# Kernel optimization log

Measured on AMD Instinct MI355X. Metric: run time of the kernel, lower is better.

Reference implementation:

```python
import jax, jax.numpy as jnp
import numpy as np

B, C_IN, H, W = 2, 256, 64, 64
D, NH, WS = 128, 8, 8          # embed_dim, num_heads, window_size
N_PTS = 8192
CAP = 256                      # max tokens per window (64 pixels + points, padded)
ODE_STEPS = 4                  # fixed-step RK4 approximating dopri5 on t in [0,1]


def setup_inputs() -> dict:
    key = jax.random.key(0)
    ks = jax.random.split(key, 16)
    p = lambda k, shape, fan: (jax.random.normal(k, shape, jnp.float32) / np.float32(np.sqrt(fan)))
    return {
        "in_image_feat": jax.random.normal(ks[0], (B, C_IN, H, W), jnp.float32),
        "pts_uv": jax.random.randint(ks[1], (N_PTS, 3), 0, 64),
        "pts_feat": jax.random.normal(ks[2], (N_PTS, D), jnp.float32),
        "conv_in_w": p(ks[3], (D, C_IN), C_IN),         # conv256_128 (1x1)
        "conv_in_b": jnp.zeros((D,), jnp.float32),
        "qkv_w": p(ks[4], (3 * D, D), D),               # sptr attn qkv
        "qkv_b": jnp.zeros((3 * D,), jnp.float32),
        "attnproj_w": p(ks[5], (D, D), D),              # sptr attn out proj
        "attnproj_b": jnp.zeros((D,), jnp.float32),
        "ode_w": p(ks[6], (D, D), D),                   # outimagefc128_128_ode
        "ode_b": jnp.zeros((D,), jnp.float32),
        "conv_out_w": p(ks[7], (C_IN, D), D),           # conv128_256 (1x1)
        "conv_out_b": jnp.zeros((C_IN,), jnp.float32),
    }


def _windowed_attention(feat, wid, NW, qkv_w, qkv_b, proj_w, proj_b):
    """Var-length windowed MHSA (sptr.VarLengthMultiheadSA) via pad-to-CAP."""
    T, d = feat.shape
    hd = d // NH
    order = jnp.argsort(wid)                      # stable sort by window id
    wid_s, feat_s = wid[order], feat[order]
    counts = jax.ops.segment_sum(jnp.ones_like(wid), wid, num_segments=NW)
    starts = jnp.cumsum(counts) - counts
    rank = jnp.arange(T) - starts[wid_s]          # within-window position
    valid = rank < CAP
    wid_w = jnp.where(valid, wid_s, NW)           # overflow -> dummy window
    rank_w = jnp.where(valid, rank, 0)
    buf = jnp.zeros((NW + 1, CAP, d), feat.dtype).at[wid_w, rank_w].set(feat_s)
    msk = jnp.zeros((NW + 1, CAP), bool).at[wid_w, rank_w].set(valid)
    qkv = buf @ qkv_w.T + qkv_b                   # [NW+1, CAP, 3d]
    q, k, v = (t.reshape(NW + 1, CAP, NH, hd) for t in jnp.split(qkv, 3, axis=-1))
    scores = jnp.einsum('wqhd,wkhd->whqk', q, k) / np.float32(np.sqrt(hd))
    scores = jnp.where(msk[:, None, None, :], scores, jnp.float32(-1e9))
    attn = jax.nn.softmax(scores, axis=-1)
    o = jnp.einsum('whqk,wkhd->wqhd', attn, v).reshape(NW + 1, CAP, d)
    o = o @ proj_w.T + proj_b
    out_s = jnp.where(valid[:, None], o[wid_w, rank_w], feat_s)
    return jnp.zeros_like(out_s).at[order].set(out_s)  # unsort


def reference(in_image_feat, pts_uv, pts_feat, conv_in_w, conv_in_b,
              qkv_w, qkv_b, attnproj_w, attnproj_b,
              ode_w, ode_b, conv_out_w, conv_out_b):
    b, c, h, w = in_image_feat.shape
    d = conv_in_w.shape[0]
    # 1x1 conv 256->128
    x = jnp.einsum('bchw,ec->bhwe', in_image_feat, conv_in_w) + conv_in_b
    pix_feat = x.reshape(b * h * w, d)
    # pixel uv grid (convert_image_to_uv): flatten order (b, h, w); u=w idx, v=h idx
    vv, uu = jnp.meshgrid(jnp.arange(h), jnp.arange(w), indexing='ij')
    pix_b = jnp.repeat(jnp.arange(b), h * w)
    pix_u = jnp.tile(uu.reshape(-1), b)
    pix_v = jnp.tile(vv.reshape(-1), b)
    # projected point uv (convert_pts_to_uv result, made in-range)
    pts_b = pts_uv[:, 0] % b
    pts_u = pts_uv[:, 1] % w
    pts_v = pts_uv[:, 2] % h
    tok_b = jnp.concatenate([pix_b, pts_b])
    tok_u = jnp.concatenate([pix_u, pts_u])
    tok_v = jnp.concatenate([pix_v, pts_v])
    feat = jnp.concatenate([pix_feat, pts_feat], axis=0)
    nwx, nwy = w // WS, h // WS
    wid = (tok_b * nwy + tok_v // WS) * nwx + tok_u // WS
    NW = b * nwx * nwy
    out = _windowed_attention(feat, wid, NW, qkv_w, qkv_b, attnproj_w, attnproj_b)
    img = out[: b * h * w]
    # fcode branch: odeint(ODEFunc(Linear), t=[0,1]) ~ fixed-step RK4, + residual
    f = lambda y: jax.nn.relu(y @ ode_w.T + ode_b)
    dt = jnp.float32(1.0 / ODE_STEPS)
    y = img
    for _ in range(ODE_STEPS):
        k1 = f(y); k2 = f(y + 0.5 * dt * k1); k3 = f(y + 0.5 * dt * k2); k4 = f(y + dt * k3)
        y = y + (dt / 6.0) * (k1 + 2.0 * k2 + 2.0 * k3 + k4)
    img = y + img
    # 1x1 conv 128->256 back to image layout
    img = img.reshape(b, h, w, d)
    return jnp.einsum('bhwd,cd->bchw', img, conv_out_w) + conv_out_b[None, :, None, None]
```

## Files before the change

kernel.cpp:

```cpp
#include <hip/hip_runtime.h>

typedef short bf16x8 __attribute__((ext_vector_type(8)));
typedef float f32x4 __attribute__((ext_vector_type(4)));

__device__ __forceinline__ float b2f(unsigned short s) {
    union { float f; unsigned u; } x; x.u = ((unsigned)s) << 16; return x.f;
}
__device__ __forceinline__ unsigned short f2b(float f) {
    unsigned u = __float_as_uint(f);
    unsigned r = (u + 0x7fffu + ((u >> 16) & 1u)) >> 16;
    return (unsigned short)r;
}

__global__ __launch_bounds__(256) void cast_k(const float* __restrict__ ciw,
                                              const float* __restrict__ qw,
                                              const float* __restrict__ pw,
                                              const float* __restrict__ ow,
                                              const float* __restrict__ cw,
                                              unsigned short* __restrict__ dst,
                                              int* __restrict__ cnt) {
    if (blockIdx.x == 0 && threadIdx.x < 128) cnt[threadIdx.x] = 0;
    int i = blockIdx.x * 256 + threadIdx.x;
    float v;
    if (i < 32768)        v = ciw[i];
    else if (i < 81920)   v = qw[i - 32768];
    else if (i < 98304)   v = pw[i - 81920];
    else if (i < 114688)  v = ow[i - 98304];
    else                  v = cw[i - 114688];
    dst[i] = f2b(v);
}

__global__ __launch_bounds__(256) void assign_k(const int* __restrict__ uv,
                                                int* __restrict__ cnt,
                                                int* __restrict__ wpts) {
    int i = blockIdx.x * 256 + threadIdx.x;
    if (i >= 8192) return;
    int b = uv[3 * i] & 1;
    int u = uv[3 * i + 1] & 63;
    int v = uv[3 * i + 2] & 63;
    int w = b * 64 + ((v >> 3) << 3) + (u >> 3);
    int slot = atomicAdd(cnt + w, 1);
    if (slot < 192) wpts[w * 192 + slot] = i;
}

__global__ __launch_bounds__(256) void cin_k(const float* __restrict__ in,
                                             const unsigned short* __restrict__ Wm,
                                             const float* __restrict__ bias,
                                             unsigned short* __restrict__ feat) {
    __shared__ unsigned short t[64][65];
    __shared__ unsigned short At[64][264];
    int p0 = blockIdx.x * 64, b = p0 >> 12, hw0 = p0 & 4095;
    int lane = threadIdx.x & 63, quad = threadIdx.x >> 6;
    for (int j = 0; j < 4; ++j) {
        int c0 = j * 64;
#pragma unroll
        for (int i = 0; i < 16; ++i) {
            int c = quad + i * 4;
            t[c][lane] = f2b(in[((size_t)(b * 256 + c0 + c)) * 4096 + hw0 + lane]);
        }
        __syncthreads();
#pragma unroll
        for (int i = 0; i < 16; ++i) {
            int p = quad + i * 4;
            At[p][c0 + lane] = t[lane][p];
        }
        __syncthreads();
    }
    int q = lane & 15, g = lane >> 4;
    int m0 = quad * 16;
    f32x4 acc[8];
#pragma unroll
    for (int tn = 0; tn < 8; ++tn) acc[tn] = (f32x4){0.f, 0.f, 0.f, 0.f};
#pragma unroll
    for (int k0 = 0; k0 < 256; k0 += 32) {
        bf16x8 a = *(const bf16x8*)&At[m0 + q][k0 + g * 8];
#pragma unroll
        for (int tn = 0; tn < 8; ++tn) {
            bf16x8 bfr = *(const bf16x8*)(Wm + (size_t)(tn * 16 + q) * 256 + k0 + g * 8);
            acc[tn] = __builtin_amdgcn_mfma_f32_16x16x32_bf16(a, bfr, acc[tn], 0, 0, 0);
        }
    }
#pragma unroll
    for (int tn = 0; tn < 8; ++tn) {
        int n = tn * 16 + q;
        float bs = bias[n];
#pragma unroll
        for (int rr = 0; rr < 4; ++rr)
            feat[(size_t)(p0 + m0 + g * 4 + rr) * 128 + n] = f2b(acc[tn][rr] + bs);
    }
}

__global__ __launch_bounds__(256) void qkv_k(const unsigned short* __restrict__ feat,
                                             const float* __restrict__ ptsf,
                                             const unsigned short* __restrict__ Wm,
                                             const float* __restrict__ bias,
                                             unsigned short* __restrict__ qkv) {
    int lane = threadIdx.x & 63, wv = threadIdx.x >> 6;
    int m0 = (blockIdx.x * 4 + wv) * 16;
    int q = lane & 15, g = lane >> 4;
    int nb = blockIdx.y * 64, koff = g * 8;
    bool isPt = m0 >= 8192;
    f32x4 acc[4];
#pragma unroll
    for (int tt = 0; tt < 4; ++tt) acc[tt] = (f32x4){0.f, 0.f, 0.f, 0.f};
#pragma unroll
    for (int k0 = 0; k0 < 128; k0 += 32) {
        bf16x8 a;
        if (isPt) {
            const float* pr = ptsf + (size_t)(m0 + q - 8192) * 128 + k0 + koff;
            float4 f0 = *(const float4*)pr;
            float4 f1 = *(const float4*)(pr + 4);
            a[0] = (short)f2b(f0.x); a[1] = (short)f2b(f0.y);
            a[2] = (short)f2b(f0.z); a[3] = (short)f2b(f0.w);
            a[4] = (short)f2b(f1.x); a[5] = (short)f2b(f1.y);
            a[6] = (short)f2b(f1.z); a[7] = (short)f2b(f1.w);
        } else {
            a = *(const bf16x8*)(feat + (size_t)(m0 + q) * 128 + k0 + koff);
        }
#pragma unroll
        for (int tt = 0; tt < 4; ++tt) {
            bf16x8 bfr = *(const bf16x8*)(Wm + (size_t)(nb + tt * 16 + q) * 128 + k0 + koff);
            acc[tt] = __builtin_amdgcn_mfma_f32_16x16x32_bf16(a, bfr, acc[tt], 0, 0, 0);
        }
    }
#pragma unroll
    for (int tt = 0; tt < 4; ++tt) {
        int n = nb + tt * 16 + q;
        float bs = bias[n];
#pragma unroll
        for (int rr = 0; rr < 4; ++rr)
            qkv[(size_t)(m0 + g * 4 + rr) * 384 + n] = f2b(acc[tt][rr] + bs);
    }
}

__global__ __launch_bounds__(256) void attn_k(const unsigned short* __restrict__ qkv,
                                              const int* __restrict__ cnt,
                                              const int* __restrict__ wpts,
                                              unsigned short* __restrict__ aout) {
    __shared__ unsigned short Kl[256][24];
    __shared__ unsigned short Vt[16][264];
    int blk = blockIdx.x;
    int w = blk >> 3, h = blk & 7;
    int b = w >> 6, wy = (w >> 3) & 7, wx = w & 7;
    int tid = threadIdx.x, wave = tid >> 6, lane = tid & 63;
    int q = lane & 15, g = lane >> 4;
    int c = cnt[w]; if (c > 192) c = 192;
    int T = 64 + c;
    {
        int t = tid;
        if (t < T) {
            int tok;
            if (t < 64) tok = b * 4096 + (wy * 8 + (t >> 3)) * 64 + wx * 8 + (t & 7);
            else        tok = 8192 + wpts[w * 192 + t - 64];
            const unsigned short* base = qkv + (size_t)tok * 384 + h * 16;
            bf16x8 k0 = *(const bf16x8*)(base + 128);
            bf16x8 v0 = *(const bf16x8*)(base + 256);
            *(bf16x8*)&Kl[t][0] = k0;
#pragma unroll
            for (int d = 0; d < 8; ++d) Vt[d][t] = (unsigned short)v0[d];
            bf16x8 k1 = *(const bf16x8*)(base + 136);
            bf16x8 v1 = *(const bf16x8*)(base + 264);
            *(bf16x8*)&Kl[t][8] = k1;
#pragma unroll
            for (int d = 0; d < 8; ++d) Vt[8 + d][t] = (unsigned short)v1[d];
        } else {
            bf16x8 z;
#pragma unroll
            for (int d = 0; d < 8; ++d) z[d] = 0;
            *(bf16x8*)&Kl[t][0] = z;
            *(bf16x8*)&Kl[t][8] = z;
#pragma unroll
            for (int d = 0; d < 16; ++d) Vt[d][t] = 0;
        }
    }
    int qq = wave * 16 + q;
    int qrow = b * 4096 + (wy * 8 + (qq >> 3)) * 64 + wx * 8 + (qq & 7);
    bf16x8 qfrag;
#pragma unroll
    for (int j = 0; j < 8; ++j) qfrag[j] = 0;
    if (g < 2) qfrag = *(const bf16x8*)(qkv + (size_t)qrow * 384 + h * 16 + g * 8);

    __syncthreads();

    float p[16][4];
    int MT = (T + 15) >> 4;
#pragma unroll
    for (int mt = 0; mt < 16; ++mt) {
        if (mt < MT) {
            bf16x8 af = *(const bf16x8*)&Kl[mt * 16 + q][(g & 1) * 8];
            f32x4 cc = (f32x4){0.f, 0.f, 0.f, 0.f};
            cc = __builtin_amdgcn_mfma_f32_16x16x32_bf16(af, qfrag, cc, 0, 0, 0);
#pragma unroll
            for (int r = 0; r < 4; ++r) {
                int tok = mt * 16 + g * 4 + r;
                p[mt][r] = (tok < T) ? cc[r] * 0.25f : -1e30f;
            }
        } else {
#pragma unroll
            for (int r = 0; r < 4; ++r) p[mt][r] = -1e30f;
        }
    }
    float mv = -3.0e38f;
#pragma unroll
    for (int mt = 0; mt < 16; ++mt)
#pragma unroll
        for (int r = 0; r < 4; ++r) mv = fmaxf(mv, p[mt][r]);
    mv = fmaxf(mv, __shfl_xor(mv, 16));
    mv = fmaxf(mv, __shfl_xor(mv, 32));
    float ls = 0.f;
#pragma unroll
    for (int mt = 0; mt < 16; ++mt)
#pragma unroll
        for (int r = 0; r < 4; ++r) {
            float e = __expf(p[mt][r] - mv);
            p[mt][r] = e;
            ls += e;
        }
    ls += __shfl_xor(ls, 16);
    ls += __shfl_xor(ls, 32);

    f32x4 oacc = (f32x4){0.f, 0.f, 0.f, 0.f};
    int KS = (T + 31) >> 5;
    int srcA = q + (((2 * g) & 3) << 4);
    int srcB = q + (((2 * g + 1) & 3) << 4);
#pragma unroll
    for (int ks = 0; ks < 8; ++ks) {
        if (ks < KS) {
            int n0lo, n0hi, n1lo, n1hi;
            asm("v_cvt_pk_bf16_f32 %0, %1, %2" : "=v"(n0lo) : "v"(p[2 * ks][0]), "v"(p[2 * ks][1]));
            asm("v_cvt_pk_bf16_f32 %0, %1, %2" : "=v"(n0hi) : "v"(p[2 * ks][2]), "v"(p[2 * ks][3]));
            asm("v_cvt_pk_bf16_f32 %0, %1, %2" : "=v"(n1lo) : "v"(p[2 * ks + 1][0]), "v"(p[2 * ks + 1][1]));
            asm("v_cvt_pk_bf16_f32 %0, %1, %2" : "=v"(n1hi) : "v"(p[2 * ks + 1][2]), "v"(p[2 * ks + 1][3]));
            int a0 = __shfl(n0lo, srcA), b0 = __shfl(n1lo, srcA);
            int a1 = __shfl(n0hi, srcA), b1 = __shfl(n1hi, srcA);
            int a2 = __shfl(n0lo, srcB), b2 = __shfl(n1lo, srcB);
            int a3 = __shfl(n0hi, srcB), b3 = __shfl(n1hi, srcB);
            union { int d[4]; bf16x8 v; } pb;
            bool lo2 = (g < 2);
            pb.d[0] = lo2 ? a0 : b0;
            pb.d[1] = lo2 ? a1 : b1;
            pb.d[2] = lo2 ? a2 : b2;
            pb.d[3] = lo2 ? a3 : b3;
            bf16x8 vf = *(const bf16x8*)&Vt[q][ks * 32 + g * 8];
            oacc = __builtin_amdgcn_mfma_f32_16x16x32_bf16(vf, pb.v, oacc, 0, 0, 0);
        }
    }
    float inv = 1.0f / ls;
    ushort4 st;
    st.x = f2b(oacc[0] * inv);
    st.y = f2b(oacc[1] * inv);
    st.z = f2b(oacc[2] * inv);
    st.w = f2b(oacc[3] * inv);
    *(ushort4*)(aout + (size_t)qrow * 128 + h * 16 + g * 4) = st;
}

__global__ __launch_bounds__(128) void tail_k(const unsigned short* __restrict__ aout,
                                              const unsigned short* __restrict__ pwb,
                                              const float* __restrict__ pb,
                                              const unsigned short* __restrict__ owb,
                                              const float* __restrict__ ob,
                                              const unsigned short* __restrict__ cwb,
                                              const float* __restrict__ cb,
                                              float* __restrict__ outp) {
    __shared__ unsigned short Wl[128][136];
    __shared__ unsigned short tc[2][16][136];
    int tid = threadIdx.x, wave = tid >> 6, lane = tid & 63;
    int g = lane >> 4, q = lane & 15;
    {
        int part = tid & 15;
#pragma unroll
        for (int it = 0; it < 16; ++it) {
            int rr = (tid >> 4) + it * 8;
            *(bf16x8*)&Wl[rr][part * 8] = *(const bf16x8*)(owb + rr * 128 + part * 8);
        }
    }
    int R0 = blockIdx.x * 32 + wave * 16;

    float y0[32];
    {
        const unsigned short* Arow = aout + (size_t)(R0 + q) * 128;
        f32x4 pacc[8];
#pragma unroll
        for (int tn = 0; tn < 8; ++tn) pacc[tn] = (f32x4){0.f, 0.f, 0.f, 0.f};
#pragma unroll
        for (int k0 = 0; k0 < 128; k0 += 32) {
            bf16x8 a = *(const bf16x8*)(Arow + k0 + g * 8);
#pragma unroll
            for (int tn = 0; tn < 8; ++tn) {
                bf16x8 bfr = *(const bf16x8*)(pwb + (size_t)(tn * 16 + q) * 128 + k0 + g * 8);
                pacc[tn] = __builtin_amdgcn_mfma_f32_16x16x32_bf16(a, bfr, pacc[tn], 0, 0, 0);
            }
        }
#pragma unroll
        for (int tn = 0; tn < 8; ++tn) {
            float bs = pb[tn * 16 + q];
#pragma unroll
            for (int rr = 0; rr < 4; ++rr) y0[tn * 4 + rr] = pacc[tn][rr] + bs;
        }
    }

    float bs[8];
#pragma unroll
    for (int tn = 0; tn < 8; ++tn) bs[tn] = ob[tn * 16 + q];
    float y[32], acc[32], ko[32];
#pragma unroll
    for (int i = 0; i < 32; ++i) y[i] = y0[i];

#define WRITE_TC(EXPR)                                            \
    {                                                             \
        _Pragma("unroll")                                         \
        for (int tn = 0; tn < 8; ++tn) {                          \
            _Pragma("unroll")                                     \
            for (int rr = 0; rr < 4; ++rr) {                      \
                int i_ = tn * 4 + rr;                             \
                tc[wave][g * 4 + rr][tn * 16 + q] = f2b(EXPR);    \
            }                                                     \
        }                                                         \
        __syncthreads();                                          \
    }

#define EVAL()                                                                         \
    {                                                                                  \
        bf16x8 af[4];                                                                  \
        _Pragma("unroll")                                                              \
        for (int tk = 0; tk < 4; ++tk)                                                 \
            af[tk] = *(const bf16x8*)&tc[wave][q][tk * 32 + g * 8];                    \
        _Pragma("unroll")                                                              \
        for (int tn = 0; tn < 8; ++tn) {                                               \
            f32x4 cc = (f32x4){0.f, 0.f, 0.f, 0.f};                                    \
            _Pragma("unroll")                                                          \
            for (int tk = 0; tk < 4; ++tk) {                                           \
                bf16x8 bfr = *(const bf16x8*)&Wl[tn * 16 + q][tk * 32 + g * 8];        \
                cc = __builtin_amdgcn_mfma_f32_16x16x32_bf16(af[tk], bfr, cc, 0, 0, 0);\
            }                                                                          \
            _Pragma("unroll")                                                          \
            for (int rr = 0; rr < 4; ++rr)                                             \
                ko[tn * 4 + rr] = fmaxf(cc[rr] + bs[tn], 0.f);                         \
        }                                                                              \
    }

    WRITE_TC(y[i_])
    const float dt = 0.25f;
    for (int st = 0; st < 4; ++st) {
        EVAL();
#pragma unroll
        for (int i = 0; i < 32; ++i) acc[i] = y[i] + (dt / 6.f) * ko[i];
        WRITE_TC(y[i_] + (0.5f * dt) * ko[i_])
        EVAL();
#pragma unroll
        for (int i = 0; i < 32; ++i) acc[i] += (dt / 3.f) * ko[i];
        WRITE_TC(y[i_] + (0.5f * dt) * ko[i_])
        EVAL();
#pragma unroll
        for (int i = 0; i < 32; ++i) acc[i] += (dt / 3.f) * ko[i];
        WRITE_TC(y[i_] + dt * ko[i_])
        EVAL();
#pragma unroll
        for (int i = 0; i < 32; ++i) y[i] = acc[i] + (dt / 6.f) * ko[i];
        WRITE_TC(y[i_])
    }

    WRITE_TC(y[i_] + y0[i_])
    {
        int p = R0 + g * 4;
        int bb = p >> 12, plo = p & 4095;
#pragma unroll
        for (int tn2 = 0; tn2 < 16; ++tn2) {
            f32x4 cc = (f32x4){0.f, 0.f, 0.f, 0.f};
#pragma unroll
            for (int tk = 0; tk < 4; ++tk) {
                bf16x8 af = *(const bf16x8*)&tc[wave][q][tk * 32 + g * 8];
                bf16x8 bfr = *(const bf16x8*)(cwb + (size_t)(tn2 * 16 + q) * 128 + tk * 32 + g * 8);
                cc = __builtin_amdgcn_mfma_f32_16x16x32_bf16(af, bfr, cc, 0, 0, 0);
            }
            int ch = tn2 * 16 + q;
            float bsv = cb[ch];
            float4 stv;
            stv.x = cc[0] + bsv;
            stv.y = cc[1] + bsv;
            stv.z = cc[2] + bsv;
            stv.w = cc[3] + bsv;
            *(float4*)(outp + ((size_t)(bb * 256 + ch)) * 4096 + plo) = stv;
        }
    }
#undef WRITE_TC
#undef EVAL
}

extern "C" void kernel_launch(void* const* d_in, const int* in_sizes, int n_in,
                              void* d_out, int out_size, void* d_ws, size_t ws_size,
                              hipStream_t stream) {
    (void)in_sizes; (void)n_in; (void)out_size; (void)ws_size;
    const float* img_in = (const float*)d_in[0];
    const int*   pts_uv = (const int*)d_in[1];
    const float* ptsf   = (const float*)d_in[2];
    const float* ciw    = (const float*)d_in[3];
    const float* cib    = (const float*)d_in[4];
    const float* qw     = (const float*)d_in[5];
    const float* qb     = (const float*)d_in[6];
    const float* pw     = (const float*)d_in[7];
    const float* pb     = (const float*)d_in[8];
    const float* ow     = (const float*)d_in[9];
    const float* ob     = (const float*)d_in[10];
    const float* cw     = (const float*)d_in[11];
    const float* cb     = (const float*)d_in[12];

    char* ws = (char*)d_ws;
    unsigned short* feat = (unsigned short*)(ws);
    unsigned short* qkv  = (unsigned short*)(ws + 2097152);
    unsigned short* aout = (unsigned short*)(ws + 14680064);
    int*            cnt  = (int*)(ws + 16777216);
    int*            wpts = (int*)(ws + 16777728);
    unsigned short* wb   = (unsigned short*)(ws + 16876544);
    unsigned short* ciw_b = wb;
    unsigned short* qw_b  = wb + 32768;
    unsigned short* pw_b  = wb + 81920;
    unsigned short* ow_b  = wb + 98304;
    unsigned short* cw_b  = wb + 114688;

    cast_k<<<576, 256, 0, stream>>>(ciw, qw, pw, ow, cw, wb, cnt);
    assign_k<<<32, 256, 0, stream>>>(pts_uv, cnt, wpts);
    cin_k<<<128, 256, 0, stream>>>(img_in, ciw_b, cib, feat);
    qkv_k<<<dim3(256, 6), 256, 0, stream>>>(feat, ptsf, qw_b, qb, qkv);
    attn_k<<<1024, 256, 0, stream>>>(qkv, cnt, wpts, aout);
    tail_k<<<256, 128, 0, stream>>>(aout, pw_b, pb, ow_b, ob, cw_b, cb, (float*)d_out);
}
```

Baseline: 170.8 us.

## Split tail kernel columns across waves and skip unused point-token query projection

The tail kernel now has both waves of a block work on the same 16 rows, each computing half of the output columns. The RK4 stage input is ping-ponged between two shared tiles. This doubles the grid size and halves the per-thread register arrays, aiming for better occupancy and parallelism, at the cost of a block-wide sync per stage. The QKV kernel also exits early for blocks that would compute query vectors for point tokens, whose outputs are never used.

```diff
diff --git a/kernel.cpp b/kernel.cpp
--- a/kernel.cpp
+++ b/kernel.cpp
@@ -95,6 +95,7 @@
                                              const unsigned short* __restrict__ Wm,
                                              const float* __restrict__ bias,
                                              unsigned short* __restrict__ qkv) {
+    if (blockIdx.x >= 128 && blockIdx.y < 2) return;
     int lane = threadIdx.x & 63, wv = threadIdx.x >> 6;
     int m0 = (blockIdx.x * 4 + wv) * 16;
     int q = lane & 15, g = lane >> 4;
@@ -274,102 +275,104 @@
             *(bf16x8*)&Wl[rr][part * 8] = *(const bf16x8*)(owb + rr * 128 + part * 8);
         }
     }
-    int R0 = blockIdx.x * 32 + wave * 16;
-
-    float y0[32];
+    int R0 = blockIdx.x * 16;
+    int tnb = wave * 4;
+
+    float y0[16];
     {
         const unsigned short* Arow = aout + (size_t)(R0 + q) * 128;
-        f32x4 pacc[8];
-#pragma unroll
-        for (int tn = 0; tn < 8; ++tn) pacc[tn] = (f32x4){0.f, 0.f, 0.f, 0.f};
+        f32x4 pacc[4];
+#pragma unroll
+        for (int t4 = 0; t4 < 4; ++t4) pacc[t4] = (f32x4){0.f, 0.f, 0.f, 0.f};
 #pragma unroll
         for (int k0 = 0; k0 < 128; k0 += 32) {
             bf16x8 a = *(const bf16x8*)(Arow + k0 + g * 8);
 #pragma unroll
-            for (int tn = 0; tn < 8; ++tn) {
-                bf16x8 bfr = *(const bf16x8*)(pwb + (size_t)(tn * 16 + q) * 128 + k0 + g * 8);
-                pacc[tn] = __builtin_amdgcn_mfma_f32_16x16x32_bf16(a, bfr, pacc[tn], 0, 0, 0);
+            for (int t4 = 0; t4 < 4; ++t4) {
+                bf16x8 bfr = *(const bf16x8*)(pwb + (size_t)((tnb + t4) * 16 + q) * 128 + k0 + g * 8);
+                pacc[t4] = __builtin_amdgcn_mfma_f32_16x16x32_bf16(a, bfr, pacc[t4], 0, 0, 0);
             }
         }
 #pragma unroll
-        for (int tn = 0; tn < 8; ++tn) {
-            float bs = pb[tn * 16 + q];
-#pragma unroll
-            for (int rr = 0; rr < 4; ++rr) y0[tn * 4 + rr] = pacc[tn][rr] + bs;
-        }
-    }
-
-    float bs[8];
-#pragma unroll
-    for (int tn = 0; tn < 8; ++tn) bs[tn] = ob[tn * 16 + q];
-    float y[32], acc[32], ko[32];
-#pragma unroll
-    for (int i = 0; i < 32; ++i) y[i] = y0[i];
-
-#define WRITE_TC(EXPR)                                            \
-    {                                                             \
-        _Pragma("unroll")                                         \
-        for (int tn = 0; tn < 8; ++tn) {                          \
-            _Pragma("unroll")                                     \
-            for (int rr = 0; rr < 4; ++rr) {                      \
-                int i_ = tn * 4 + rr;                             \
-                tc[wave][g * 4 + rr][tn * 16 + q] = f2b(EXPR);    \
-            }                                                     \
-        }                                                         \
-        __syncthreads();                                          \
-    }
-
-#define EVAL()                                                                         \
+        for (int t4 = 0; t4 < 4; ++t4) {
+            float bsv = pb[(tnb + t4) * 16 + q];
+#pragma unroll
+            for (int rr = 0; rr < 4; ++rr) y0[t4 * 4 + rr] = pacc[t4][rr] + bsv;
+        }
+    }
+
+    float bs[4];
+#pragma unroll
+    for (int t4 = 0; t4 < 4; ++t4) bs[t4] = ob[(tnb + t4) * 16 + q];
+    float y[16], ac[16], ko[16];
+#pragma unroll
+    for (int i = 0; i < 16; ++i) y[i] = y0[i];
+
+#define WRITE_TC(BUF, EXPR)                                               \
+    {                                                                     \
+        _Pragma("unroll")                                                 \
+        for (int t4 = 0; t4 < 4; ++t4) {                                  \
+            _Pragma("unroll")                                             \
+            for (int rr = 0; rr < 4; ++rr) {                              \
+                int i_ = t4 * 4 + rr;                                     \
+                tc[BUF][g * 4 + rr][(tnb + t4) * 16 + q] = f2b(EXPR);     \
+            }                                                             \
+        }                                                                 \
+        __syncthreads();                                                  \
+    }
+
+#define EVAL(BUF)                                                                      \
     {                                                                                  \
         bf16x8 af[4];                                                                  \
         _Pragma("unroll")                                                              \
         for (int tk = 0; tk < 4; ++tk)                                                 \
-            af[tk] = *(const bf16x8*)&tc[wave][q][tk * 32 + g * 8];                    \
+            af[tk] = *(const bf16x8*)&tc[BUF][q][tk * 32 + g * 8];                     \
         _Pragma("unroll")                                                              \
-        for (int tn = 0; tn < 8; ++tn) {                                               \
+        for (int t4 = 0; t4 < 4; ++t4) {                                               \
             f32x4 cc = (f32x4){0.f, 0.f, 0.f, 0.f};                                    \
             _Pragma("unroll")                                                          \
             for (int tk = 0; tk < 4; ++tk) {                                           \
-                bf16x8 bfr = *(const bf16x8*)&Wl[tn * 16 + q][tk * 32 + g * 8];        \
+                bf16x8 bfr = *(const bf16x8*)&Wl[(tnb + t4) * 16 + q][tk * 32 + g * 8];\
                 cc = __builtin_amdgcn_mfma_f32_16x16x32_bf16(af[tk], bfr, cc, 0, 0, 0);\
             }                                                                          \
             _Pragma("unroll")                                                          \
             for (int rr = 0; rr < 4; ++rr)                                             \
-                ko[tn * 4 + rr] = fmaxf(cc[rr] + bs[tn], 0.f);                         \
+                ko[t4 * 4 + rr] = fmaxf(cc[rr] + bs[t4], 0.f);                         \
         }                                                                              \
     }
 
-    WRITE_TC(y[i_])
+    WRITE_TC(0, y[i_])
     const float dt = 0.25f;
     for (int st = 0; st < 4; ++st) {
-        EVAL();
-#pragma unroll
-        for (int i = 0; i < 32; ++i) acc[i] = y[i] + (dt / 6.f) * ko[i];
-        WRITE_TC(y[i_] + (0.5f * dt) * ko[i_])
-        EVAL();
-#pragma unroll
-        for (int i = 0; i < 32; ++i) acc[i] += (dt / 3.f) * ko[i];
-        WRITE_TC(y[i_] + (0.5f * dt) * ko[i_])
-        EVAL();
-#pragma unroll
-        for (int i = 0; i < 32; ++i) acc[i] += (dt / 3.f) * ko[i];
-        WRITE_TC(y[i_] + dt * ko[i_])
-        EVAL();
-#pragma unroll
-        for (int i = 0; i < 32; ++i) y[i] = acc[i] + (dt / 6.f) * ko[i];
-        WRITE_TC(y[i_])
-    }
-
-    WRITE_TC(y[i_] + y0[i_])
+        EVAL(0);
+#pragma unroll
+        for (int i = 0; i < 16; ++i) ac[i] = y[i] + (dt / 6.f) * ko[i];
+        WRITE_TC(1, y[i_] + (0.5f * dt) * ko[i_])
+        EVAL(1);
+#pragma unroll
+        for (int i = 0; i < 16; ++i) ac[i] += (dt / 3.f) * ko[i];
+        WRITE_TC(0, y[i_] + (0.5f * dt) * ko[i_])
+        EVAL(0);
+#pragma unroll
+        for (int i = 0; i < 16; ++i) ac[i] += (dt / 3.f) * ko[i];
+        WRITE_TC(1, y[i_] + dt * ko[i_])
+        EVAL(1);
+#pragma unroll
+        for (int i = 0; i < 16; ++i) y[i] = ac[i] + (dt / 6.f) * ko[i];
+        WRITE_TC(0, y[i_])
+    }
+
+    WRITE_TC(1, y[i_] + y0[i_])
     {
         int p = R0 + g * 4;
         int bb = p >> 12, plo = p & 4095;
 #pragma unroll
-        for (int tn2 = 0; tn2 < 16; ++tn2) {
+        for (int t2 = 0; t2 < 8; ++t2) {
+            int tn2 = wave * 8 + t2;
             f32x4 cc = (f32x4){0.f, 0.f, 0.f, 0.f};
 #pragma unroll
             for (int tk = 0; tk < 4; ++tk) {
-                bf16x8 af = *(const bf16x8*)&tc[wave][q][tk * 32 + g * 8];
+                bf16x8 af = *(const bf16x8*)&tc[1][q][tk * 32 + g * 8];
                 bf16x8 bfr = *(const bf16x8*)(cwb + (size_t)(tn2 * 16 + q) * 128 + tk * 32 + g * 8);
                 cc = __builtin_amdgcn_mfma_f32_16x16x32_bf16(af, bfr, cc, 0, 0, 0);
             }
@@ -423,5 +426,5 @@
     cin_k<<<128, 256, 0, stream>>>(img_in, ciw_b, cib, feat);
     qkv_k<<<dim3(256, 6), 256, 0, stream>>>(feat, ptsf, qw_b, qb, qkv);
     attn_k<<<1024, 256, 0, stream>>>(qkv, cnt, wpts, aout);
-    tail_k<<<256, 128, 0, stream>>>(aout, pw_b, pb, ow_b, ob, cw_b, cb, (float*)d_out);
-}
+    tail_k<<<512, 128, 0, stream>>>(aout, pw_b, pb, ow_b, ob, cw_b, cb, (float*)d_out);
+}
```

Result: faster. 153.4 us (-10.2%).
